# Optimization experiments

Hardware: AMD Instinct MI355X
Metric: run time of the kernel (lower is better)

Reference implementation:

```python
import jax, jax.numpy as jnp
from jax import lax
import numpy as np

# Dims: batch, input channels (=3*C), output channels, kernel size, spatial
B, CIN, C, K, H, W = 8, 576, 192, 3, 56, 56
KK = K * K  # number of kernel positions


def setup_inputs() -> dict:
    key = jax.random.key(0)
    k1, k2, k3, k4 = jax.random.split(key, 4)
    x = jax.random.normal(k1, (B, CIN, H, W), jnp.float32)
    # 1x1 conv producing per-channel, per-position dynamic logits (C*KK outputs)
    fc_w = jax.random.normal(k2, (C * KK, CIN), jnp.float32) * 0.05
    # per-position grouped conv kernels: (KK, C_out, CIN//C=3, K, K)
    w1 = jax.random.normal(k3, (KK, C, CIN // C, K, K), jnp.float32) * 0.1
    # per-position depthwise conv kernels: (KK, C, K, K)
    w2 = jax.random.normal(k4, (KK, C, K, K), jnp.float32) * 0.1
    return {"x": x, "fc_w": fc_w, "w1": w1, "w2": w2}


def reference(x, fc_w, w1, w2):
    b = x.shape[0]
    # dynamic softmax weights over the KK kernel positions: (b, C, KK, H, W)
    logits = jnp.einsum('oc,bchw->bohw', fc_w, x).reshape(b, C, KK, H, W)
    attn = jax.nn.softmax(logits, axis=2)

    # dep_conv1: per-position grouped conv (3C -> C, groups=C), vmapped over KK
    def conv1(wi):  # wi: (C, 3, K, K)
        return lax.conv_general_dilated(x, wi, (1, 1), 'SAME',
                                        feature_group_count=C)

    feat = jax.nn.relu(jax.vmap(conv1)(w1))  # (KK, b, C, H, W)

    # dep_conv2: per-position depthwise conv (C -> C, groups=C)
    def conv2(fi, wi):  # fi: (b, C, H, W), wi: (C, K, K)
        return lax.conv_general_dilated(fi, wi[:, None], (1, 1), 'SAME',
                                        feature_group_count=C)

    out_pos = jax.vmap(conv2)(feat, w2)  # (KK, b, C, H, W)

    # softmax-weighted aggregation over kernel positions
    out = jnp.einsum('ibchw,bcihw->bchw', out_pos, attn)  # (b, C, H, W)
    return out
```

## Files before the change

kernel.cpp:

```cpp
#include <hip/hip_runtime.h>
#include <hip/hip_bf16.h>

constexpr int Bn   = 8;
constexpr int Cin  = 576;
constexpr int Cc   = 192;
constexpr int Hh   = 56;
constexpr int Ww   = 56;
constexpr int HWn  = Hh * Ww;
constexpr int CKK  = Cc * 9;

constexpr int GM = 1792;
constexpr int GK = 576;
constexpr int GN = Bn * HWn;

using f16x8 = __attribute__((ext_vector_type(8))) _Float16;
using f32x4 = __attribute__((ext_vector_type(4))) float;

__device__ __forceinline__ void async_copy16(void* lds, const void* gptr) {
    __builtin_amdgcn_global_load_lds(
        (const __attribute__((address_space(1))) unsigned int*)gptr,
        (__attribute__((address_space(3))) unsigned int*)lds, 16, 0, 0);
}

__device__ __forceinline__ float blo(unsigned int u) { return __uint_as_float(u << 16); }
__device__ __forceinline__ float bhi(unsigned int u) { return __uint_as_float(u & 0xffff0000u); }

__global__ __launch_bounds__(256) void cast_fcw_kernel(
    const float* __restrict__ fcw, _Float16* __restrict__ out)
{
    int idx = blockIdx.x * 256 + threadIdx.x;
    int e = idx * 4;
    if (e >= GM * GK) return;
    int row = e / GK;
    union { ushort4 u; _Float16 h[4]; } pk;
    if (row < CKK) {
        float4 v = *(const float4*)&fcw[e];
        pk.h[0] = (_Float16)v.x; pk.h[1] = (_Float16)v.y;
        pk.h[2] = (_Float16)v.z; pk.h[3] = (_Float16)v.w;
    } else {
        pk.h[0] = pk.h[1] = pk.h[2] = pk.h[3] = (_Float16)0.f;
    }
    *(ushort4*)&out[e] = pk.u;
}

__global__ __launch_bounds__(256) void transpose_cast_kernel(
    const float* __restrict__ x, _Float16* __restrict__ xt)
{
    __shared__ float t[32][65];
    const int b = blockIdx.z, k0 = blockIdx.y * 32, hw0 = blockIdx.x * 64;
    const int tid = threadIdx.x;
    const int col = tid & 63, kr = tid >> 6;
#pragma unroll
    for (int p = 0; p < 8; p++) {
        int k = kr + p * 4;
        t[k][col] = x[(size_t)(b * Cin + k0 + k) * HWn + hw0 + col];
    }
    __syncthreads();
    const int row = tid >> 2, cq = (tid & 3) * 8;
    union { uint4 u; _Float16 h[8]; } pk;
#pragma unroll
    for (int j = 0; j < 8; j++) pk.h[j] = (_Float16)t[cq + j][row];
    *(uint4*)&xt[(size_t)(b * HWn + hw0 + row) * GK + k0 + cq] = pk.u;
}

__global__ __launch_bounds__(256) void gemm_mfma_kernel(
    const _Float16* __restrict__ A, const _Float16* __restrict__ Bm,
    __hip_bfloat16* __restrict__ logits)
{
    __shared__ _Float16 As[128 * 32];
    __shared__ _Float16 Bs[128 * 32];

    const int tid = threadIdx.x;
    const int n0 = blockIdx.x * 128;
    const int m0 = blockIdx.y * 128;
    const int lane = tid & 63;
    const int wave = tid >> 6;
    const int wm = (wave >> 1) * 64;
    const int wn = (wave & 1) * 64;
    const int lm = lane & 15;
    const int kq = (lane >> 4) * 8;

    const int r0 = tid >> 2;
    const int c0 = (tid & 3) * 8;

    f32x4 acc[4][4] = {};

    for (int k0 = 0; k0 < GK; k0 += 32) {
        async_copy16(&As[r0 * 32 + c0],        &A[(size_t)(m0 + r0) * GK + k0 + c0]);
        async_copy16(&As[(64 + r0) * 32 + c0], &A[(size_t)(m0 + 64 + r0) * GK + k0 + c0]);
        async_copy16(&Bs[r0 * 32 + c0],        &Bm[(size_t)(n0 + r0) * GK + k0 + c0]);
        async_copy16(&Bs[(64 + r0) * 32 + c0], &Bm[(size_t)(n0 + 64 + r0) * GK + k0 + c0]);
        __syncthreads();
        f16x8 af[4], bf[4];
#pragma unroll
        for (int i = 0; i < 4; i++) {
            af[i] = *(const f16x8*)&As[(wm + i * 16 + lm) * 32 + kq];
            bf[i] = *(const f16x8*)&Bs[(wn + i * 16 + lm) * 32 + kq];
        }
#pragma unroll
        for (int i = 0; i < 4; i++)
#pragma unroll
            for (int j = 0; j < 4; j++)
                acc[i][j] = __builtin_amdgcn_mfma_f32_16x16x32_f16(af[i], bf[j], acc[i][j], 0, 0, 0);
        __syncthreads();
    }

#pragma unroll
    for (int j = 0; j < 4; j++) {
        int n = n0 + wn + j * 16 + lm;
        int b = n / HWn, hw = n % HWn;
#pragma unroll
        for (int i = 0; i < 4; i++) {
            int mbase = m0 + wm + i * 16 + (lane >> 4) * 4;
#pragma unroll
            for (int r = 0; r < 4; r++) {
                int m = mbase + r;
                if (m < CKK)
                    logits[((size_t)b * CKK + m) * HWn + hw] = __float2bfloat16(acc[i][j][r]);
            }
        }
    }
}

__global__ __launch_bounds__(256, 3) void conv1_kernel(
    const float* __restrict__ x, const float* __restrict__ w1,
    __hip_bfloat16* __restrict__ feat)
{
    const int c = blockIdx.x, hb = blockIdx.y, b = blockIdx.z;
    const int tid = threadIdx.x;
    const int h0 = hb * 28;
    __shared__ float xt[3][30][60];

    for (int idx = tid; idx < 1260; idx += 256) {
        int d = idx / 420, rem = idx - d * 420;
        int r = rem / 14, g = rem - r * 14;
        int h = h0 - 1 + r;
        float4 v = {0.f, 0.f, 0.f, 0.f};
        if (h >= 0 && h < Hh)
            v = *(const float4*)&x[((size_t)(b * Cin + 3 * c + d) * Hh + h) * Ww + 4 * g];
        xt[d][r][1 + 4 * g + 0] = v.x;
        xt[d][r][1 + 4 * g + 1] = v.y;
        xt[d][r][1 + 4 * g + 2] = v.z;
        xt[d][r][1 + 4 * g + 3] = v.w;
    }
    for (int idx = tid; idx < 180; idx += 256) {
        int d = idx / 60, rem = idx - d * 60;
        int r = rem >> 1, col = (rem & 1) ? 57 : 0;
        xt[d][r][col] = 0.f;
    }
    __syncthreads();

    if (tid < 224) {
        const int row = tid >> 3, seg = tid & 7;
        const int w0 = seg * 7;

        float win[3][3][9];
#pragma unroll
        for (int d = 0; d < 3; d++)
#pragma unroll
            for (int u = 0; u < 3; u++)
#pragma unroll
                for (int k = 0; k < 9; k++)
                    win[d][u][k] = xt[d][row + u][w0 + k];

        const int hw = (h0 + row) * Ww + w0;
#pragma unroll 1
        for (int i = 0; i < 9; i++) {
            const float* wp = w1 + ((size_t)i * Cc + c) * 27;
            float wgt[27];
#pragma unroll
            for (int j = 0; j < 27; j++) wgt[j] = wp[j];
            float acc[7] = {};
#pragma unroll
            for (int d = 0; d < 3; d++)
#pragma unroll
                for (int u = 0; u < 3; u++)
#pragma unroll
                    for (int v = 0; v < 3; v++) {
                        float wv = wgt[d * 9 + u * 3 + v];
#pragma unroll
                        for (int p = 0; p < 7; p++)
                            acc[p] += win[d][u][p + v] * wv;
                    }
            __hip_bfloat16* fp = feat + (((size_t)i * Bn + b) * Cc + c) * HWn + hw;
#pragma unroll
            for (int p = 0; p < 7; p++)
                fp[p] = __float2bfloat16(fmaxf(acc[p], 0.f));
        }
    }
}

__global__ __launch_bounds__(256, 3) void conv2_agg_kernel(
    const __hip_bfloat16* __restrict__ feat,
    const __hip_bfloat16* __restrict__ logits,
    const float* __restrict__ w2, float* __restrict__ out)
{
    const int c = blockIdx.x, hb = blockIdx.y, b = blockIdx.z;
    const int tid = threadIdx.x;
    const int h0 = hb * 28;
    __shared__ unsigned short ft[9][30][72];

    for (int idx = tid; idx < 1890; idx += 256) {
        int i = idx / 210, rem = idx - i * 210;
        int r = rem / 7, g = rem - r * 7;
        int h = h0 - 1 + r;
        uint4 v = {0u, 0u, 0u, 0u};
        if (h >= 0 && h < Hh)
            v = *(const uint4*)&feat[(((size_t)i * Bn + b) * Cc + c) * HWn + h * Ww + 8 * g];
        unsigned int* dst = (unsigned int*)&ft[i][r][2 + 8 * g];
        dst[0] = v.x; dst[1] = v.y; dst[2] = v.z; dst[3] = v.w;
    }
    for (int idx = tid; idx < 1080; idx += 256) {
        int i = idx / 120, rem = idx - i * 120;
        int r = rem >> 2, e = rem & 3;
        int col = (e < 2) ? e : 56 + e;
        ft[i][r][col] = 0;
    }
    __syncthreads();

    if (tid < 196) {
        const int row = tid / 7, seg = tid - row * 7;
        const int w0 = 8 * seg;
        const int hw = (h0 + row) * Ww + w0;

        float lg[9][8];
        const __hip_bfloat16* lbase = logits + ((size_t)b * CKK + c * 9) * HWn + hw;
#pragma unroll
        for (int i = 0; i < 9; i++) {
            uint4 lv = *(const uint4*)&lbase[(size_t)i * HWn];
            lg[i][0] = blo(lv.x); lg[i][1] = bhi(lv.x);
            lg[i][2] = blo(lv.y); lg[i][3] = bhi(lv.y);
            lg[i][4] = blo(lv.z); lg[i][5] = bhi(lv.z);
            lg[i][6] = blo(lv.w); lg[i][7] = bhi(lv.w);
        }
        float mx[8], sum[8];
#pragma unroll
        for (int p = 0; p < 8; p++) {
            mx[p] = lg[0][p];
#pragma unroll
            for (int i = 1; i < 9; i++) mx[p] = fmaxf(mx[p], lg[i][p]);
            sum[p] = 0.f;
        }
#pragma unroll
        for (int i = 0; i < 9; i++)
#pragma unroll
            for (int p = 0; p < 8; p++) {
                lg[i][p] = __expf(lg[i][p] - mx[p]);
                sum[p] += lg[i][p];
            }

        float oacc[8] = {};
#pragma unroll
        for (int i = 0; i < 9; i++) {
            const float* wp = w2 + ((size_t)i * Cc + c) * 9;
            float wgt[9];
#pragma unroll
            for (int j = 0; j < 9; j++) wgt[j] = wp[j];
            float cacc[8] = {};
#pragma unroll
            for (int u = 0; u < 3; u++) {
                const unsigned short* fr = &ft[i][row + u][w0];
                uint4 a = *(const uint4*)fr;
                uint2 bq = *(const uint2*)(fr + 8);
                float wf[11];
                wf[1] = bhi(a.x);
                wf[2] = blo(a.y);  wf[3] = bhi(a.y);
                wf[4] = blo(a.z);  wf[5] = bhi(a.z);
                wf[6] = blo(a.w);  wf[7] = bhi(a.w);
                wf[8] = blo(bq.x); wf[9] = bhi(bq.x);
                wf[10] = blo(bq.y);
#pragma unroll
                for (int v = 0; v < 3; v++) {
                    float wv = wgt[u * 3 + v];
#pragma unroll
                    for (int p = 0; p < 8; p++)
                        cacc[p] += wf[p + v + 1] * wv;
                }
            }
#pragma unroll
            for (int p = 0; p < 8; p++) oacc[p] += cacc[p] * lg[i][p];
        }

        float* obase = out + ((size_t)(b * Cc + c)) * HWn + hw;
        float4 o0, o1;
        o0.x = oacc[0] * __builtin_amdgcn_rcpf(sum[0]);
        o0.y = oacc[1] * __builtin_amdgcn_rcpf(sum[1]);
        o0.z = oacc[2] * __builtin_amdgcn_rcpf(sum[2]);
        o0.w = oacc[3] * __builtin_amdgcn_rcpf(sum[3]);
        o1.x = oacc[4] * __builtin_amdgcn_rcpf(sum[4]);
        o1.y = oacc[5] * __builtin_amdgcn_rcpf(sum[5]);
        o1.z = oacc[6] * __builtin_amdgcn_rcpf(sum[6]);
        o1.w = oacc[7] * __builtin_amdgcn_rcpf(sum[7]);
        *(float4*)&obase[0] = o0;
        *(float4*)&obase[4] = o1;
    }
}

extern "C" void kernel_launch(void* const* d_in, const int* in_sizes, int n_in,
                              void* d_out, int out_size, void* d_ws, size_t ws_size,
                              hipStream_t stream)
{
    const float* x    = (const float*)d_in[0];
    const float* fc_w = (const float*)d_in[1];
    const float* w1   = (const float*)d_in[2];
    const float* w2   = (const float*)d_in[3];
    float* out = (float*)d_out;

    char* ws = (char*)d_ws;
    __hip_bfloat16* logits = (__hip_bfloat16*)ws;
    char* region2 = ws + (size_t)Bn * CKK * HWn * 2;
    __hip_bfloat16* feat = (__hip_bfloat16*)region2;
    _Float16* xt    = (_Float16*)region2;
    _Float16* fcw16 = (_Float16*)(region2 + (size_t)GN * GK * 2);

    cast_fcw_kernel<<<(GM * GK / 4 + 255) / 256, 256, 0, stream>>>(fc_w, fcw16);
    transpose_cast_kernel<<<dim3(HWn / 64, GK / 32, Bn), 256, 0, stream>>>(x, xt);
    gemm_mfma_kernel<<<dim3(GN / 128, GM / 128), 256, 0, stream>>>(fcw16, xt, logits);
    conv1_kernel<<<dim3(Cc, 2, Bn), 256, 0, stream>>>(x, w1, feat);
    conv2_agg_kernel<<<dim3(Cc, 2, Bn), 256, 0, stream>>>(feat, logits, w2, out);
}
```

Before: 292.3 us.

## Swizzle GEMM LDS, transpose MFMA for vector logits stores, vectorize conv1 feat stores

The GEMM now XOR-swizzles its LDS layout to reduce bank conflicts on fragment reads. It also swaps the MFMA operand order so each lane holds four consecutive spatial outputs, which allows packed 8-byte bf16 stores of the logits instead of scattered 2-byte stores. conv1 is remapped so each thread computes eight outputs and writes them as one 16-byte packed bf16 store. The conv2 position loop is set to unroll 1, which lowers register pressure but may cost instruction-level parallelism.

```diff
diff --git a/kernel.cpp b/kernel.cpp
--- a/kernel.cpp
+++ b/kernel.cpp
@@ -24,6 +24,9 @@
 
 __device__ __forceinline__ float blo(unsigned int u) { return __uint_as_float(u << 16); }
 __device__ __forceinline__ float bhi(unsigned int u) { return __uint_as_float(u & 0xffff0000u); }
+__device__ __forceinline__ unsigned short bf16bits(float f) {
+    union { __hip_bfloat16 h; unsigned short u; } c; c.h = __float2bfloat16(f); return c.u;
+}
 
 __global__ __launch_bounds__(256) void cast_fcw_kernel(
     const float* __restrict__ fcw, _Float16* __restrict__ out)
@@ -78,46 +81,55 @@
     const int wm = (wave >> 1) * 64;
     const int wn = (wave & 1) * 64;
     const int lm = lane & 15;
-    const int kq = (lane >> 4) * 8;
-
-    const int r0 = tid >> 2;
-    const int c0 = (tid & 3) * 8;
+    const int lc = lane >> 4;
+
+    const int lrow = tid >> 2;
+    const int koff = (((tid & 3) ^ ((tid >> 3) & 3)) << 3);
+
+    int offA[4], offB[4];
+#pragma unroll
+    for (int i = 0; i < 4; i++) {
+        int ra = wm + i * 16 + lm;
+        offA[i] = ra * 32 + ((lc ^ ((ra >> 1) & 3)) << 3);
+        int rb = wn + i * 16 + lm;
+        offB[i] = rb * 32 + ((lc ^ ((rb >> 1) & 3)) << 3);
+    }
 
     f32x4 acc[4][4] = {};
 
     for (int k0 = 0; k0 < GK; k0 += 32) {
-        async_copy16(&As[r0 * 32 + c0],        &A[(size_t)(m0 + r0) * GK + k0 + c0]);
-        async_copy16(&As[(64 + r0) * 32 + c0], &A[(size_t)(m0 + 64 + r0) * GK + k0 + c0]);
-        async_copy16(&Bs[r0 * 32 + c0],        &Bm[(size_t)(n0 + r0) * GK + k0 + c0]);
-        async_copy16(&Bs[(64 + r0) * 32 + c0], &Bm[(size_t)(n0 + 64 + r0) * GK + k0 + c0]);
+        async_copy16(&As[(size_t)tid * 8],        &A[(size_t)(m0 + lrow) * GK + k0 + koff]);
+        async_copy16(&As[2048 + (size_t)tid * 8], &A[(size_t)(m0 + 64 + lrow) * GK + k0 + koff]);
+        async_copy16(&Bs[(size_t)tid * 8],        &Bm[(size_t)(n0 + lrow) * GK + k0 + koff]);
+        async_copy16(&Bs[2048 + (size_t)tid * 8], &Bm[(size_t)(n0 + 64 + lrow) * GK + k0 + koff]);
         __syncthreads();
         f16x8 af[4], bf[4];
 #pragma unroll
         for (int i = 0; i < 4; i++) {
-            af[i] = *(const f16x8*)&As[(wm + i * 16 + lm) * 32 + kq];
-            bf[i] = *(const f16x8*)&Bs[(wn + i * 16 + lm) * 32 + kq];
+            af[i] = *(const f16x8*)&As[offA[i]];
+            bf[i] = *(const f16x8*)&Bs[offB[i]];
         }
 #pragma unroll
         for (int i = 0; i < 4; i++)
 #pragma unroll
             for (int j = 0; j < 4; j++)
-                acc[i][j] = __builtin_amdgcn_mfma_f32_16x16x32_f16(af[i], bf[j], acc[i][j], 0, 0, 0);
+                acc[i][j] = __builtin_amdgcn_mfma_f32_16x16x32_f16(bf[j], af[i], acc[i][j], 0, 0, 0);
         __syncthreads();
     }
 
-#pragma unroll
-    for (int j = 0; j < 4; j++) {
-        int n = n0 + wn + j * 16 + lm;
-        int b = n / HWn, hw = n % HWn;
-#pragma unroll
-        for (int i = 0; i < 4; i++) {
-            int mbase = m0 + wm + i * 16 + (lane >> 4) * 4;
-#pragma unroll
-            for (int r = 0; r < 4; r++) {
-                int m = mbase + r;
-                if (m < CKK)
-                    logits[((size_t)b * CKK + m) * HWn + hw] = __float2bfloat16(acc[i][j][r]);
-            }
+    const int mcol = m0 + wm + lm;
+#pragma unroll
+    for (int i = 0; i < 4; i++) {
+        int m = mcol + i * 16;
+        if (m >= CKK) continue;
+#pragma unroll
+        for (int j = 0; j < 4; j++) {
+            int n = n0 + wn + j * 16 + lc * 4;
+            int b = n / HWn, hw = n - b * HWn;
+            uint2 pk;
+            pk.x = (unsigned)bf16bits(acc[i][j][0]) | ((unsigned)bf16bits(acc[i][j][1]) << 16);
+            pk.y = (unsigned)bf16bits(acc[i][j][2]) | ((unsigned)bf16bits(acc[i][j][3]) << 16);
+            *(uint2*)&logits[((size_t)b * CKK + m) * HWn + hw] = pk;
         }
     }
 }
@@ -150,17 +162,17 @@
     }
     __syncthreads();
 
-    if (tid < 224) {
-        const int row = tid >> 3, seg = tid & 7;
-        const int w0 = seg * 7;
-
-        float win[3][3][9];
+    if (tid < 196) {
+        const int row = tid / 7, seg = tid - (tid / 7) * 7;
+        const int w0 = seg * 8;
+
+        float win[3][3][10];
 #pragma unroll
         for (int d = 0; d < 3; d++)
 #pragma unroll
             for (int u = 0; u < 3; u++)
 #pragma unroll
-                for (int k = 0; k < 9; k++)
+                for (int k = 0; k < 10; k++)
                     win[d][u][k] = xt[d][row + u][w0 + k];
 
         const int hw = (h0 + row) * Ww + w0;
@@ -170,7 +182,7 @@
             float wgt[27];
 #pragma unroll
             for (int j = 0; j < 27; j++) wgt[j] = wp[j];
-            float acc[7] = {};
+            float acc[8] = {};
 #pragma unroll
             for (int d = 0; d < 3; d++)
 #pragma unroll
@@ -179,13 +191,15 @@
                     for (int v = 0; v < 3; v++) {
                         float wv = wgt[d * 9 + u * 3 + v];
 #pragma unroll
-                        for (int p = 0; p < 7; p++)
+                        for (int p = 0; p < 8; p++)
                             acc[p] += win[d][u][p + v] * wv;
                     }
-            __hip_bfloat16* fp = feat + (((size_t)i * Bn + b) * Cc + c) * HWn + hw;
-#pragma unroll
-            for (int p = 0; p < 7; p++)
-                fp[p] = __float2bfloat16(fmaxf(acc[p], 0.f));
+            uint4 pk;
+            pk.x = (unsigned)bf16bits(fmaxf(acc[0], 0.f)) | ((unsigned)bf16bits(fmaxf(acc[1], 0.f)) << 16);
+            pk.y = (unsigned)bf16bits(fmaxf(acc[2], 0.f)) | ((unsigned)bf16bits(fmaxf(acc[3], 0.f)) << 16);
+            pk.z = (unsigned)bf16bits(fmaxf(acc[4], 0.f)) | ((unsigned)bf16bits(fmaxf(acc[5], 0.f)) << 16);
+            pk.w = (unsigned)bf16bits(fmaxf(acc[6], 0.f)) | ((unsigned)bf16bits(fmaxf(acc[7], 0.f)) << 16);
+            *(uint4*)&feat[(((size_t)i * Bn + b) * Cc + c) * HWn + hw] = pk;
         }
     }
 }
@@ -219,7 +233,7 @@
     __syncthreads();
 
     if (tid < 196) {
-        const int row = tid / 7, seg = tid - row * 7;
+        const int row = tid / 7, seg = tid - (tid / 7) * 7;
         const int w0 = 8 * seg;
         const int hw = (h0 + row) * Ww + w0;
 
@@ -250,7 +264,7 @@
             }
 
         float oacc[8] = {};
-#pragma unroll
+#pragma unroll 1
         for (int i = 0; i < 9; i++) {
             const float* wp = w2 + ((size_t)i * Cc + c) * 9;
             float wgt[9];
```

New measurement: 446.7 us. +52.8%, slower.
